# Kernel tuning notes

Measured on AMD Instinct MI355X. Metric: run time of the kernel, lower is better.

The kernel has to match this reference:

```python
import jax, jax.numpy as jnp
import numpy as np

D_MODEL = 1024
D_STATE = 16
D_CONV = 4
EXPAND = 2
D_INNER = D_MODEL * EXPAND
BATCH = 4
SEQ_LEN = 4096


def setup_inputs() -> dict:
    key = jax.random.key(0)
    ks = jax.random.split(key, 6)
    def rn(k, shape, scale):
        return jax.random.normal(k, shape, dtype=jnp.float32) * scale
    x = rn(ks[0], (BATCH, SEQ_LEN, D_MODEL), 1.0)
    in_proj_w = rn(ks[1], (2 * D_INNER, D_MODEL), D_MODEL ** -0.5)
    conv_w = rn(ks[2], (D_INNER, 1, D_CONV), D_CONV ** -0.5)  # depthwise conv kernel
    conv_b = rn(ks[3], (D_INNER,), 0.02)
    x_proj_w = rn(ks[4], (2 * D_STATE + 1, D_INNER), D_INNER ** -0.5)
    A_log = jnp.log(jnp.arange(1, D_STATE + 1, dtype=jnp.float32))  # module's init
    D = jnp.ones((D_INNER,), jnp.float32)
    out_proj_w = rn(ks[5], (D_MODEL, D_INNER), D_INNER ** -0.5)
    return dict(x=x, in_proj_w=in_proj_w, conv_w=conv_w, conv_b=conv_b,
                x_proj_w=x_proj_w, A_log=A_log, D=D, out_proj_w=out_proj_w)


def _silu(v):
    return v * jax.nn.sigmoid(v)


def reference(x, in_proj_w, conv_w, conv_b, x_proj_w, A_log, D, out_proj_w):
    b, l, _ = x.shape
    # input projection -> (b, l, 2*d_inner), split into x_inner and gate z
    xz = jnp.einsum('bld,ed->ble', x, in_proj_w)
    x_inner, z = jnp.split(xz, 2, axis=-1)
    # causal depthwise conv1d: torch pads both sides d_conv-1 then truncates to l,
    # equivalent to left-pad d_conv-1 only
    xc = jnp.transpose(x_inner, (0, 2, 1))  # (b, d_inner, l)
    xc = jax.lax.conv_general_dilated(
        xc, conv_w, window_strides=(1,), padding=[(D_CONV - 1, 0)],
        feature_group_count=D_INNER, dimension_numbers=('NCH', 'OIH', 'NCH'))
    xc = xc + conv_b[None, :, None]
    x_conv = _silu(jnp.transpose(xc, (0, 2, 1)))  # (b, l, d_inner)
    # SSM parameter projection: [delta(1) | B(d_state) | C(d_state)]
    x_dbl = jnp.einsum('bld,ed->ble', x_conv, x_proj_w)
    delta = jax.nn.softplus(x_dbl[..., 0])       # (b, l) scalar per token
    B_ssm = x_dbl[..., 1:D_STATE + 1]            # (b, l, n)
    C_ssm = x_dbl[..., D_STATE + 1:]             # (b, l, n)
    A = -jnp.exp(A_log)                          # (n,)

    def step(h, inp):
        x_t, d_t, B_t, C_t = inp  # (b,d_inner), (b,), (b,n), (b,n)
        dA = jnp.exp(d_t[:, None, None] * A)          # (b, 1, n)
        dB = d_t[:, None, None] * B_t[:, None, :]     # (b, 1, n)
        h = h * dA + x_t[:, :, None] * dB             # (b, d_inner, n)
        y_t = jnp.einsum('bdn,bn->bd', h, C_t)
        return h, y_t

    h0 = jnp.zeros((b, D_INNER, D_STATE), x.dtype)
    xs = (jnp.swapaxes(x_conv, 0, 1), jnp.swapaxes(delta, 0, 1),
          jnp.swapaxes(B_ssm, 0, 1), jnp.swapaxes(C_ssm, 0, 1))
    _, ys = jax.lax.scan(step, h0, xs)  # ys: (l, b, d_inner)
    y = jnp.swapaxes(ys, 0, 1)
    y = y + x_conv * D
    y = y * _silu(z)
    return jnp.einsum('bld,od->blo', y, out_proj_w)
```

## Files before the change

### kernel.cpp

```cpp
#include <hip/hip_runtime.h>
#include <hip/hip_fp16.h>

typedef _Float16 f16;
typedef _Float16 half8 __attribute__((ext_vector_type(8)));
typedef _Float16 half4v __attribute__((ext_vector_type(4)));
typedef float f32x4 __attribute__((ext_vector_type(4)));

#define AS1(p) ((const __attribute__((address_space(1))) void*)(p))
#define AS3(p) ((__attribute__((address_space(3))) void*)(p))

__device__ __forceinline__ void gload_lds16(const void* g, void* l) {
    __builtin_amdgcn_global_load_lds(AS1(g), AS3(l), 16, 0, 0);
}

__global__ __launch_bounds__(256)
void prep_k(const float* __restrict__ x, const float* __restrict__ w_in,
            const float* __restrict__ w_xp,
            f16* __restrict__ xh, f16* __restrict__ wih, f16* __restrict__ Wh) {
    int b = blockIdx.x;
    if (b < 2048) {
        for (int i = b * 256 + threadIdx.x; i < 4194304; i += 2048 * 256) {
            float4 v = ((const float4*)x)[i];
            half4v o; o[0] = (f16)v.x; o[1] = (f16)v.y; o[2] = (f16)v.z; o[3] = (f16)v.w;
            ((half4v*)xh)[i] = o;
        }
    } else if (b < 2560) {
        for (int i = (b - 2048) * 256 + threadIdx.x; i < 1048576; i += 512 * 256) {
            float4 v = ((const float4*)w_in)[i];
            half4v o; o[0] = (f16)v.x; o[1] = (f16)v.y; o[2] = (f16)v.z; o[3] = (f16)v.w;
            ((half4v*)wih)[i] = o;
        }
    } else {
        int idx = (b - 2560) * 256 + threadIdx.x;
        int e = idx >> 11;
        int k = idx & 2047;
        Wh[idx] = (e < 33) ? (f16)w_xp[e * 2048 + k] : (f16)0.f;
    }
}

__global__ __launch_bounds__(256) void cvt_f16_k(const float* __restrict__ in,
                                                 f16* __restrict__ out, int n4) {
    for (int i = blockIdx.x * 256 + threadIdx.x; i < n4; i += gridDim.x * 256) {
        float4 v = ((const float4*)in)[i];
        half4v o;
        o[0] = (f16)v.x; o[1] = (f16)v.y; o[2] = (f16)v.z; o[3] = (f16)v.w;
        ((half4v*)out)[i] = o;
    }
}

__device__ __forceinline__ void stage_q(const f16* __restrict__ g, int ld,
                                        int row0, int gk, f16* q,
                                        int tid, int wave) {
#pragma unroll
    for (int rd = 0; rd < 2; ++rd) {
        int t = rd * 512 + tid;
        int r = t >> 2;
        int cu = (t & 3) ^ ((r >> 1) & 3);
        gload_lds16(g + (size_t)(row0 + r) * ld + gk + cu * 8,
                    q + rd * 4096 + wave * 512);
    }
}

#define PH(Q, KH, MH, LOADB, STAGE, WAITC)                                    \
  {                                                                           \
    half8 afr[4];                                                             \
    {                                                                         \
      const f16* aq = &lds[Q][0][KH][0];                                      \
      int ra = wm * 128 + (MH) * 64 + lr;                                     \
      afr[0] = *(const half8*)(aq + (ra +  0) * 32 + cofs);                   \
      afr[1] = *(const half8*)(aq + (ra + 16) * 32 + cofs);                   \
      afr[2] = *(const half8*)(aq + (ra + 32) * 32 + cofs);                   \
      afr[3] = *(const half8*)(aq + (ra + 48) * 32 + cofs);                   \
    }                                                                         \
    if (LOADB) {                                                              \
      const f16* bq = &lds[Q][1][KH][0];                                      \
      int rb = wn * 64 + lr;                                                  \
      bfr[0] = *(const half8*)(bq + (rb +  0) * 32 + cofs);                   \
      bfr[1] = *(const half8*)(bq + (rb + 16) * 32 + cofs);                   \
      bfr[2] = *(const half8*)(bq + (rb + 32) * 32 + cofs);                   \
      bfr[3] = *(const half8*)(bq + (rb + 48) * 32 + cofs);                   \
    }                                                                         \
    STAGE;                                                                    \
    __builtin_amdgcn_s_barrier();                                             \
    asm volatile("s_waitcnt lgkmcnt(0)" ::: "memory");                        \
    __builtin_amdgcn_sched_barrier(0);                                        \
    __builtin_amdgcn_s_setprio(1);                                            \
    _Pragma("unroll")                                                         \
    for (int f_ = 0; f_ < 4; ++f_)                                            \
      _Pragma("unroll")                                                       \
      for (int j_ = 0; j_ < 4; ++j_)                                          \
        acc[(MH) * 4 + f_][j_] = __builtin_amdgcn_mfma_f32_16x16x32_f16(      \
            afr[f_], bfr[j_], acc[(MH) * 4 + f_][j_], 0, 0, 0);               \
    __builtin_amdgcn_s_setprio(0);                                            \
    __builtin_amdgcn_sched_barrier(0);                                        \
    WAITC;                                                                    \
    __builtin_amdgcn_s_barrier();                                             \
  }

template <typename OutT, int NT>
__global__ __launch_bounds__(512, 2)
void gemm8p_pers(const f16* __restrict__ A, const f16* __restrict__ B,
                 OutT* __restrict__ C, int N, int K, int lda, int ldc) {
    __shared__ f16 lds[2][2][2][8192];

    int nTn = N >> 8;
    unsigned grid = gridDim.x;
    unsigned cpx = (grid * (unsigned)NT) >> 3;

    int tid = threadIdx.x;
    int wave = tid >> 6;
    int lane = tid & 63;
    int wm = wave >> 2;
    int wn = wave & 3;
    int lr = lane & 15;
    int cg = lane >> 4;
    int cofs = ((cg ^ ((lr >> 1) & 3)) << 3);

    f32x4 acc[8][4];
#pragma unroll
    for (int i = 0; i < 8; ++i)
#pragma unroll
        for (int j = 0; j < 4; ++j) acc[i][j] = (f32x4){0.f, 0.f, 0.f, 0.f};
    half8 bfr[4];

    auto tileMN = [&](int j, int& tm, int& tn) {
        unsigned o = blockIdx.x + grid * (unsigned)j;
        unsigned s = (o & 7u) * cpx + (o >> 3);
        tm = (int)(s / (unsigned)nTn) * 256;
        tn = (int)(s % (unsigned)nTn) * 256;
    };

    int bm, bn;
    tileMN(0, bm, bn);

    stage_q(B, K,   bn, 0,  &lds[0][1][0][0], tid, wave);
    stage_q(A, lda, bm, 0,  &lds[0][0][0][0], tid, wave);
    stage_q(B, K,   bn, 32, &lds[0][1][1][0], tid, wave);
    stage_q(A, lda, bm, 32, &lds[0][0][1][0], tid, wave);
    stage_q(B, K,   bn, 64, &lds[1][1][0][0], tid, wave);
    stage_q(A, lda, bm, 64, &lds[1][0][0][0], tid, wave);
    stage_q(B, K,   bn, 96, &lds[1][1][1][0], tid, wave);
    asm volatile("s_waitcnt vmcnt(6)" ::: "memory");
    __builtin_amdgcn_s_barrier();

    int NI = K >> 7;
    for (int j = 0; j < NT; ++j) {
        int bm2 = bm, bn2 = bn;
        if (j + 1 < NT) tileMN(j + 1, bm2, bn2);

        for (int it = 0; it < NI; ++it) {
            int gk = it << 7;
            bool lastIter = (it == NI - 1);
            bool fin = lastIter && (j + 1 == NT);
            int sbm = lastIter ? bm2 : bm;
            int sbn = lastIter ? bn2 : bn;
            int sgk = lastIter ? 0 : gk + 128;

            PH(0, 0, 0, true,
               { stage_q(A, lda, bm, gk + 96, &lds[1][0][1][0], tid, wave); }, {});
            PH(0, 0, 1, false,
               { if (!fin) stage_q(B, K, sbn, sgk, &lds[0][1][0][0], tid, wave); }, {});
            PH(0, 1, 0, true,
               { if (!fin) stage_q(A, lda, sbm, sgk, &lds[0][0][0][0], tid, wave); }, {});
            PH(0, 1, 1, false,
               { if (!fin) stage_q(B, K, sbn, sgk + 32, &lds[0][1][1][0], tid, wave); },
               { if (fin) asm volatile("s_waitcnt vmcnt(0)" ::: "memory");
                 else     asm volatile("s_waitcnt vmcnt(6)" ::: "memory"); });
            PH(1, 0, 0, true,
               { if (!fin) stage_q(A, lda, sbm, sgk + 32, &lds[0][0][1][0], tid, wave); }, {});
            PH(1, 0, 1, false,
               { if (!fin) stage_q(B, K, sbn, sgk + 64, &lds[1][1][0][0], tid, wave); }, {});
            PH(1, 1, 0, true,
               { if (!fin) stage_q(A, lda, sbm, sgk + 64, &lds[1][0][0][0], tid, wave); }, {});
            PH(1, 1, 1, false,
               { if (!fin) stage_q(B, K, sbn, sgk + 96, &lds[1][1][1][0], tid, wave); },
               { if (!fin) asm volatile("s_waitcnt vmcnt(6)" ::: "memory"); });
        }

        int orow0 = bm + wm * 128 + (lane >> 4) * 4;
        int ocol0 = bn + wn * 64 + lr;
#pragma unroll
        for (int mf = 0; mf < 8; ++mf)
#pragma unroll
            for (int nj = 0; nj < 4; ++nj)
#pragma unroll
                for (int r = 0; r < 4; ++r)
                    C[(size_t)(orow0 + mf * 16 + r) * ldc + (ocol0 + nj * 16)] =
                        (OutT)acc[mf][nj][r];
#pragma unroll
        for (int i2 = 0; i2 < 8; ++i2)
#pragma unroll
            for (int j2 = 0; j2 < 4; ++j2) acc[i2][j2] = (f32x4){0.f, 0.f, 0.f, 0.f};
        bm = bm2; bn = bn2;
    }
}

__global__ __launch_bounds__(256, 2)
void xdbl_mfma_k(const f16* __restrict__ xc, const f16* __restrict__ Wh,
                 float* __restrict__ xdbl) {
    __shared__ f16 As[64 * 64];
    __shared__ f16 Bs[48 * 64];
    int bm = blockIdx.x * 64;
    int tid = threadIdx.x;
    int wave = tid >> 6;
    int lane = tid & 63;
    int srow = lane >> 3;
    int scol = (lane & 7) * 8;
    int lr = lane & 15;
    int lkh = (lane >> 4) * 8;

    f32x4 acc[3];
#pragma unroll
    for (int j = 0; j < 3; ++j) acc[j] = (f32x4){0.f, 0.f, 0.f, 0.f};

    for (int k0 = 0; k0 < 2048; k0 += 64) {
        __syncthreads();
#pragma unroll
        for (int i = 0; i < 2; ++i) {
            int slot = wave * 2 + i;
            gload_lds16(xc + (size_t)(bm + slot * 8 + srow) * 2048 + (k0 + scol),
                        As + slot * 512);
        }
        if (wave < 3) {
#pragma unroll
            for (int i = 0; i < 2; ++i) {
                int slot = wave * 2 + i;
                gload_lds16(Wh + (size_t)(slot * 8 + srow) * 2048 + (k0 + scol),
                            Bs + slot * 512);
            }
        }
        asm volatile("s_waitcnt vmcnt(0)" ::: "memory");
        __syncthreads();
#pragma unroll
        for (int kk = 0; kk < 2; ++kk) {
            half8 a = *(const half8*)(As + (wave * 16 + lr) * 64 + kk * 32 + lkh);
#pragma unroll
            for (int nj = 0; nj < 3; ++nj) {
                half8 b = *(const half8*)(Bs + (nj * 16 + lr) * 64 + kk * 32 + lkh);
                acc[nj] = __builtin_amdgcn_mfma_f32_16x16x32_f16(a, b, acc[nj], 0, 0, 0);
            }
        }
    }

    int orow0 = bm + wave * 16 + (lane >> 4) * 4;
#pragma unroll
    for (int nj = 0; nj < 3; ++nj) {
        int col = nj * 16 + lr;
        if (col < 33) {
#pragma unroll
            for (int r = 0; r < 4; ++r)
                xdbl[(size_t)(orow0 + r) * 33 + col] = acc[nj][r];
        }
    }
}

__global__ __launch_bounds__(256)
void conv_silu_k(const f16* __restrict__ xz, const float* __restrict__ cw,
                 const float* __restrict__ cb, f16* __restrict__ xc) {
    int r0 = blockIdx.x * 8;
    int d0 = threadIdx.x << 3;
    int l0 = r0 & 4095;

    const float4* cw4 = (const float4*)cw;
    float4 w[8];
    float bias[8];
#pragma unroll
    for (int e = 0; e < 8; ++e) { w[e] = cw4[d0 + e]; bias[e] = cb[d0 + e]; }

    half8 xv[11];
#pragma unroll
    for (int j = 0; j < 11; ++j) {
        if (l0 - 3 + j >= 0)
            xv[j] = *(const half8*)(xz + (size_t)(r0 - 3 + j) * 4096 + d0);
        else
            xv[j] = (half8){};
    }

#pragma unroll
    for (int rr = 0; rr < 8; ++rr) {
        float acc[8];
#pragma unroll
        for (int e = 0; e < 8; ++e) acc[e] = bias[e];
#pragma unroll
        for (int k = 0; k < 4; ++k) {
            half8 xk = xv[rr + k];
#pragma unroll
            for (int e = 0; e < 8; ++e) {
                float wj = (k == 0) ? w[e].x : (k == 1) ? w[e].y : (k == 2) ? w[e].z : w[e].w;
                acc[e] = fmaf((float)xk[e], wj, acc[e]);
            }
        }
        half8 out = {};
#pragma unroll
        for (int e = 0; e < 8; ++e) {
            float v = acc[e];
            out[e] = (f16)(v / (1.f + expf(-v)));
        }
        *(half8*)(xc + (size_t)(r0 + rr) * 2048 + d0) = out;
    }
}

__global__ __launch_bounds__(128)
void spg_k(const float* __restrict__ xdbl, const float* __restrict__ A_log,
           float* __restrict__ SP, float* __restrict__ G) {
    __shared__ float red[128];
    int bc = blockIdx.x;
    int t = threadIdx.x;
    int m = bc * 128 + t;
    const float* row = xdbl + (size_t)m * 33;
    float v0 = row[0];
    float d = (v0 > 15.f) ? v0 : logf(1.f + expf(v0));
    float* sp = SP + (size_t)m * 48;
#pragma unroll
    for (int n = 0; n < 16; ++n) {
        float An = -expf(A_log[n]);
        sp[n] = expf(An * d);
        sp[16 + n] = d * row[1 + n];
        sp[32 + n] = row[17 + n];
    }
    red[t] = d;
    __syncthreads();
#pragma unroll
    for (int s = 64; s > 0; s >>= 1) {
        if (t < s) red[t] += red[t + s];
        __syncthreads();
    }
    if (t < 16) G[bc * 16 + t] = expf(-expf(A_log[t]) * red[0]);
}

__global__ __launch_bounds__(256)
void scan1_k(const f16* __restrict__ xc, const float* __restrict__ SP,
             float* __restrict__ F) {
    __shared__ float sp[128 * 48];
    int blk = blockIdx.x;
    int dg = blk & 7;
    int bc = blk >> 3;
    int tid = threadIdx.x;
    int wave = tid >> 6;
    int d = dg * 256 + tid;
    int mbase = bc * 128;

    const char* spb = (const char*)(SP + (size_t)mbase * 48);
#pragma unroll
    for (int i = 0; i < 6; ++i)
        gload_lds16(spb + (size_t)(i * 256 + tid) * 16,
                    (char*)sp + (size_t)(i * 256 + wave * 64) * 16);
    asm volatile("s_waitcnt vmcnt(0)" ::: "memory");
    __syncthreads();

    float h[16];
#pragma unroll
    for (int n = 0; n < 16; ++n) h[n] = 0.f;

#pragma unroll 2
    for (int tt = 0; tt < 128; ++tt) {
        const float* r = sp + tt * 48;
        float x = (float)xc[(size_t)(mbase + tt) * 2048 + d];
#pragma unroll
        for (int n = 0; n < 16; ++n) h[n] = fmaf(h[n], r[n], x * r[16 + n]);
    }
    size_t fb = ((size_t)bc * 2048 + d) * 16;
#pragma unroll
    for (int n = 0; n < 16; ++n) F[fb + n] = h[n];
}

__global__ __launch_bounds__(256)
void combine_k(const float* __restrict__ F, const float* __restrict__ G,
               float* __restrict__ H0) {
    int gid = blockIdx.x * 256 + threadIdx.x;
    int b = gid >> 15;
    int dn = gid & 32767;
    int n = dn & 15;
    float h = 0.f;
    for (int c = 0; c < 32; ++c) {
        int bc = b * 32 + c;
        size_t idx = (size_t)bc * 32768 + dn;
        H0[idx] = h;
        h = fmaf(G[bc * 16 + n], h, F[idx]);
    }
}

__global__ __launch_bounds__(256)
void scan2_k(const f16* __restrict__ xc, const f16* xz, const float* __restrict__ SP,
             const float* __restrict__ H0, const float* __restrict__ Dv,
             f16* yout) {
    __shared__ float sp[128 * 48];
    int blk = blockIdx.x;
    int dg = blk & 7;
    int bc = blk >> 3;
    int tid = threadIdx.x;
    int wave = tid >> 6;
    int d = dg * 256 + tid;
    int mbase = bc * 128;

    const char* spb = (const char*)(SP + (size_t)mbase * 48);
#pragma unroll
    for (int i = 0; i < 6; ++i)
        gload_lds16(spb + (size_t)(i * 256 + tid) * 16,
                    (char*)sp + (size_t)(i * 256 + wave * 64) * 16);
    asm volatile("s_waitcnt vmcnt(0)" ::: "memory");
    __syncthreads();

    size_t fb = ((size_t)bc * 2048 + d) * 16;
    float h[16];
#pragma unroll
    for (int n = 0; n < 16; ++n) h[n] = H0[fb + n];
    float Dd = Dv[d];

#pragma unroll 2
    for (int tt = 0; tt < 128; ++tt) {
        const float* r = sp + tt * 48;
        size_t mrow = (size_t)(mbase + tt);
        float x = (float)xc[mrow * 2048 + d];
        float z = (float)xz[mrow * 4096 + 2048 + d];
        float y0 = 0.f, y1 = 0.f, y2 = 0.f, y3 = 0.f;
#pragma unroll
        for (int n = 0; n < 16; n += 4) {
            h[n]     = fmaf(h[n],     r[n],     x * r[16 + n]);
            h[n + 1] = fmaf(h[n + 1], r[n + 1], x * r[17 + n]);
            h[n + 2] = fmaf(h[n + 2], r[n + 2], x * r[18 + n]);
            h[n + 3] = fmaf(h[n + 3], r[n + 3], x * r[19 + n]);
            y0 = fmaf(h[n],     r[32 + n], y0);
            y1 = fmaf(h[n + 1], r[33 + n], y1);
            y2 = fmaf(h[n + 2], r[34 + n], y2);
            y3 = fmaf(h[n + 3], r[35 + n], y3);
        }
        float y = (y0 + y1) + (y2 + y3);
        float yf = fmaf(x, Dd, y);
        float sz = z / (1.f + expf(-z));
        yout[mrow * 4096 + d] = (f16)(yf * sz);
    }
}

extern "C" void kernel_launch(void* const* d_in, const int* in_sizes, int n_in,
                              void* d_out, int out_size, void* d_ws, size_t ws_size,
                              hipStream_t stream) {
    const float* x      = (const float*)d_in[0];
    const float* w_in   = (const float*)d_in[1];
    const float* conv_w = (const float*)d_in[2];
    const float* conv_b = (const float*)d_in[3];
    const float* w_xp   = (const float*)d_in[4];
    const float* A_log  = (const float*)d_in[5];
    const float* Dv     = (const float*)d_in[6];
    const float* w_out  = (const float*)d_in[7];

    char* base = (char*)d_ws;
    f16* xzh = (f16*)base;
    char* r1 = base + 134217728;
    f16* xh  = (f16*)r1;
    f16* wih = (f16*)(r1 + 33554432);
    f16* xch = (f16*)r1;
    f16* woh = (f16*)r1;
    char* p = base + 201326592;
    float* xdbl = (float*)p;  p += 2162688;
    p += 65536;
    float* SP   = (float*)p;  p += 3145728;
    float* G    = (float*)p;  p += 8192;
    float* F    = (float*)p;  p += 16777216;
    float* H0   = (float*)p;  p += 16777216;
    f16*   Wh   = (f16*)p;    p += 196608;

    prep_k<<<2944, 256, 0, stream>>>(x, w_in, w_xp, xh, wih, Wh);

    gemm8p_pers<f16, 4><<<256, 512, 0, stream>>>(xh, wih, xzh, 4096, 1024, 1024, 4096);

    conv_silu_k<<<2048, 256, 0, stream>>>(xzh, conv_w, conv_b, xch);

    xdbl_mfma_k<<<256, 256, 0, stream>>>(xch, Wh, xdbl);

    spg_k<<<128, 128, 0, stream>>>(xdbl, A_log, SP, G);

    scan1_k<<<1024, 256, 0, stream>>>(xch, SP, F);
    combine_k<<<512, 256, 0, stream>>>(F, G, H0);
    scan2_k<<<1024, 256, 0, stream>>>(xch, xzh, SP, H0, Dv, xzh);

    cvt_f16_k<<<2048, 256, 0, stream>>>(w_out, woh, 524288);

    gemm8p_pers<float, 1><<<256, 512, 0, stream>>>(xzh, woh, (float*)d_out,
                                                   1024, 2048, 4096, 1024);
}
```

Measured before the change: 446.1 us.

## Fuse SP construction into scan kernels, fold w_out conversion into prep, regroup GEMM tiles

Removes the separate spg_k kernel: each scan block now builds its softplus/exp parameter table in shared memory straight from xdbl, and scan1 also computes the chunk decay G. The w_out fp32-to-fp16 conversion moves into the prep kernel, so it gets its own workspace buffer and one launch is dropped. The GEMM tile mapping is changed to group 4 M-tiles per N column, aiming for better L2 reuse. In exchange, each of the 8 d-group blocks recomputes the same exp/softplus work redundantly.

Measured after the change: 442.3 us. Within noise of the previous version (-0.8%).

```diff
diff --git a/kernel.cpp b/kernel.cpp
--- a/kernel.cpp
+++ b/kernel.cpp
@@ -15,8 +15,9 @@
 
 __global__ __launch_bounds__(256)
 void prep_k(const float* __restrict__ x, const float* __restrict__ w_in,
-            const float* __restrict__ w_xp,
-            f16* __restrict__ xh, f16* __restrict__ wih, f16* __restrict__ Wh) {
+            const float* __restrict__ w_xp, const float* __restrict__ w_out,
+            f16* __restrict__ xh, f16* __restrict__ wih,
+            f16* __restrict__ Wh, f16* __restrict__ woh) {
     int b = blockIdx.x;
     if (b < 2048) {
         for (int i = b * 256 + threadIdx.x; i < 4194304; i += 2048 * 256) {
@@ -30,21 +31,17 @@
             half4v o; o[0] = (f16)v.x; o[1] = (f16)v.y; o[2] = (f16)v.z; o[3] = (f16)v.w;
             ((half4v*)wih)[i] = o;
         }
-    } else {
+    } else if (b < 2944) {
         int idx = (b - 2560) * 256 + threadIdx.x;
         int e = idx >> 11;
         int k = idx & 2047;
         Wh[idx] = (e < 33) ? (f16)w_xp[e * 2048 + k] : (f16)0.f;
-    }
-}
-
-__global__ __launch_bounds__(256) void cvt_f16_k(const float* __restrict__ in,
-                                                 f16* __restrict__ out, int n4) {
-    for (int i = blockIdx.x * 256 + threadIdx.x; i < n4; i += gridDim.x * 256) {
-        float4 v = ((const float4*)in)[i];
-        half4v o;
-        o[0] = (f16)v.x; o[1] = (f16)v.y; o[2] = (f16)v.z; o[3] = (f16)v.w;
-        ((half4v*)out)[i] = o;
+    } else {
+        for (int i = (b - 2944) * 256 + threadIdx.x; i < 524288; i += 512 * 256) {
+            float4 v = ((const float4*)w_out)[i];
+            half4v o; o[0] = (f16)v.x; o[1] = (f16)v.y; o[2] = (f16)v.z; o[3] = (f16)v.w;
+            ((half4v*)woh)[i] = o;
+        }
     }
 }
 
@@ -126,8 +123,11 @@
     auto tileMN = [&](int j, int& tm, int& tn) {
         unsigned o = blockIdx.x + grid * (unsigned)j;
         unsigned s = (o & 7u) * cpx + (o >> 3);
-        tm = (int)(s / (unsigned)nTn) * 256;
-        tn = (int)(s % (unsigned)nTn) * 256;
+        unsigned gnn = (unsigned)(4 * nTn);
+        unsigned g = s / gnn;
+        unsigned r = s - g * gnn;
+        tm = (int)(g * 4 + (r & 3u)) * 256;
+        tn = (int)(r >> 2) * 256;
     };
 
     int bm, bn;
@@ -300,53 +300,52 @@
     }
 }
 
-__global__ __launch_bounds__(128)
-void spg_k(const float* __restrict__ xdbl, const float* __restrict__ A_log,
-           float* __restrict__ SP, float* __restrict__ G) {
+__device__ __forceinline__ void build_sp(const float* __restrict__ xdbl,
+                                         const float* __restrict__ alog,
+                                         float* sp, float* red,
+                                         int bc, int tid) {
+    if (tid < 128) {
+        int m = bc * 128 + tid;
+        const float* row = xdbl + (size_t)m * 33;
+        float v0 = row[0];
+        float d = (v0 > 15.f) ? v0 : logf(1.f + expf(v0));
+        float* s = sp + tid * 48;
+#pragma unroll
+        for (int n = 0; n < 16; ++n) {
+            float An = -expf(alog[n]);
+            s[n] = expf(An * d);
+            s[16 + n] = d * row[1 + n];
+            s[32 + n] = row[17 + n];
+        }
+        if (red) red[tid] = d;
+    }
+}
+
+__global__ __launch_bounds__(256)
+void scan1_k(const f16* __restrict__ xc, const float* __restrict__ xdbl,
+             const float* __restrict__ A_log,
+             float* __restrict__ F, float* __restrict__ G) {
+    __shared__ float sp[128 * 48];
     __shared__ float red[128];
-    int bc = blockIdx.x;
-    int t = threadIdx.x;
-    int m = bc * 128 + t;
-    const float* row = xdbl + (size_t)m * 33;
-    float v0 = row[0];
-    float d = (v0 > 15.f) ? v0 : logf(1.f + expf(v0));
-    float* sp = SP + (size_t)m * 48;
-#pragma unroll
-    for (int n = 0; n < 16; ++n) {
-        float An = -expf(A_log[n]);
-        sp[n] = expf(An * d);
-        sp[16 + n] = d * row[1 + n];
-        sp[32 + n] = row[17 + n];
-    }
-    red[t] = d;
-    __syncthreads();
-#pragma unroll
-    for (int s = 64; s > 0; s >>= 1) {
-        if (t < s) red[t] += red[t + s];
-        __syncthreads();
-    }
-    if (t < 16) G[bc * 16 + t] = expf(-expf(A_log[t]) * red[0]);
-}
-
-__global__ __launch_bounds__(256)
-void scan1_k(const f16* __restrict__ xc, const float* __restrict__ SP,
-             float* __restrict__ F) {
-    __shared__ float sp[128 * 48];
+    __shared__ float alog[16];
     int blk = blockIdx.x;
     int dg = blk & 7;
     int bc = blk >> 3;
     int tid = threadIdx.x;
-    int wave = tid >> 6;
     int d = dg * 256 + tid;
     int mbase = bc * 128;
 
-    const char* spb = (const char*)(SP + (size_t)mbase * 48);
-#pragma unroll
-    for (int i = 0; i < 6; ++i)
-        gload_lds16(spb + (size_t)(i * 256 + tid) * 16,
-                    (char*)sp + (size_t)(i * 256 + wave * 64) * 16);
-    asm volatile("s_waitcnt vmcnt(0)" ::: "memory");
+    if (tid < 16) alog[tid] = A_log[tid];
     __syncthreads();
+    build_sp(xdbl, alog, sp, red, bc, tid);
+    __syncthreads();
+#pragma unroll
+    for (int s2 = 64; s2 > 0; s2 >>= 1) {
+        if (tid < s2) red[tid] += red[tid + s2];
+        __syncthreads();
+    }
+    if (dg == 0 && tid < 16)
+        G[bc * 16 + tid] = expf(-expf(alog[tid]) * red[0]);
 
     float h[16];
 #pragma unroll
@@ -381,24 +380,22 @@
 }
 
 __global__ __launch_bounds__(256)
-void scan2_k(const f16* __restrict__ xc, const f16* xz, const float* __restrict__ SP,
+void scan2_k(const f16* __restrict__ xc, const f16* xz,
+             const float* __restrict__ xdbl, const float* __restrict__ A_log,
              const float* __restrict__ H0, const float* __restrict__ Dv,
              f16* yout) {
     __shared__ float sp[128 * 48];
+    __shared__ float alog[16];
     int blk = blockIdx.x;
     int dg = blk & 7;
     int bc = blk >> 3;
     int tid = threadIdx.x;
-    int wave = tid >> 6;
     int d = dg * 256 + tid;
     int mbase = bc * 128;
 
-    const char* spb = (const char*)(SP + (size_t)mbase * 48);
-#pragma unroll
-    for (int i = 0; i < 6; ++i)
-        gload_lds16(spb + (size_t)(i * 256 + tid) * 16,
-                    (char*)sp + (size_t)(i * 256 + wave * 64) * 16);
-    asm volatile("s_waitcnt vmcnt(0)" ::: "memory");
+    if (tid < 16) alog[tid] = A_log[tid];
+    __syncthreads();
+    build_sp(xdbl, alog, sp, nullptr, bc, tid);
     __syncthreads();
 
     size_t fb = ((size_t)bc * 2048 + d) * 16;
@@ -450,17 +447,15 @@
     f16* xh  = (f16*)r1;
     f16* wih = (f16*)(r1 + 33554432);
     f16* xch = (f16*)r1;
-    f16* woh = (f16*)r1;
     char* p = base + 201326592;
     float* xdbl = (float*)p;  p += 2162688;
-    p += 65536;
-    float* SP   = (float*)p;  p += 3145728;
     float* G    = (float*)p;  p += 8192;
     float* F    = (float*)p;  p += 16777216;
     float* H0   = (float*)p;  p += 16777216;
     f16*   Wh   = (f16*)p;    p += 196608;
-
-    prep_k<<<2944, 256, 0, stream>>>(x, w_in, w_xp, xh, wih, Wh);
+    f16*   woh  = (f16*)p;    p += 4194304;
+
+    prep_k<<<3456, 256, 0, stream>>>(x, w_in, w_xp, w_out, xh, wih, Wh, woh);
 
     gemm8p_pers<f16, 4><<<256, 512, 0, stream>>>(xh, wih, xzh, 4096, 1024, 1024, 4096);
 
@@ -468,13 +463,9 @@
 
     xdbl_mfma_k<<<256, 256, 0, stream>>>(xch, Wh, xdbl);
 
-    spg_k<<<128, 128, 0, stream>>>(xdbl, A_log, SP, G);
-
-    scan1_k<<<1024, 256, 0, stream>>>(xch, SP, F);
+    scan1_k<<<1024, 256, 0, stream>>>(xch, xdbl, A_log, F, G);
     combine_k<<<512, 256, 0, stream>>>(F, G, H0);
-    scan2_k<<<1024, 256, 0, stream>>>(xch, xzh, SP, H0, Dv, xzh);
-
-    cvt_f16_k<<<2048, 256, 0, stream>>>(w_out, woh, 524288);
+    scan2_k<<<1024, 256, 0, stream>>>(xch, xzh, xdbl, A_log, H0, Dv, xzh);
 
     gemm8p_pers<float, 1><<<256, 512, 0, stream>>>(xzh, woh, (float*)d_out,
                                                    1024, 2048, 4096, 1024);
```
